# Optimization experiments

Measured on AMD Instinct MI355X. Metric: run time of the kernel, lower is better.

The kernel has to match this reference:

```python
import jax, jax.numpy as jnp
import numpy as np


def setup_inputs() -> dict:
    key = jax.random.key(0)
    k1, k2 = jax.random.split(key)
    N, D = 8192, 1024
    x = jax.random.normal(k1, (N, D), dtype=jnp.float32)
    w = jax.random.normal(k2, (D, 1), dtype=jnp.float32)
    return {"x": x, "w": w}


def reference(x, w):
    # x: [N, D], w: [D, 1]
    N = x.shape[0]
    a = jax.nn.sigmoid(x @ w)[:, 0]          # [N], values in (0, 1)
    b = jnp.cumsum(a)                         # [N] running sum
    idx = jnp.floor(b).astype(jnp.int32)      # bin index per column
    prev = jnp.concatenate([jnp.zeros(1, jnp.int32), idx[:-1]])
    same = idx == prev                        # did we stay in the same bin?
    frac = b - idx.astype(b.dtype)            # portion falling into bin `idx`
    cols = jnp.arange(N)
    # value written at [idx, i]: a_i if same bin, else the fractional overflow
    main_val = jnp.where(same, a, frac)
    # cross-boundary remainder written at [idx-1, i]
    cross_val = jnp.where(same, 0.0, a - frac)
    cross_row = jnp.where(same, idx, idx - 1)  # dummy (add 0) when same
    trans_mat = (
        jnp.zeros((N, N), dtype=x.dtype)
        .at[idx, cols].set(main_val)
        .at[cross_row, cols].add(cross_val)
    )
    return trans_mat @ x                      # [N, D]
```

## Files before the change

kernel.cpp:

```cpp
#include <hip/hip_runtime.h>
#include <math.h>


__global__ __launch_bounds__(256) void dot_sigmoid_kernel(
    const float* __restrict__ x, const float* __restrict__ w,
    float* __restrict__ a, double* __restrict__ blocksum,
    int* __restrict__ rowptr, int N, int D) {
  __shared__ float was[4];
  int t = threadIdx.x;
  int lane = t & 63;
  int wave = t >> 6;
  int row = blockIdx.x * 4 + wave;
  const float4* xr = reinterpret_cast<const float4*>(x + (size_t)row * D);
  const float4* w4 = reinterpret_cast<const float4*>(w);
  float acc = 0.f;
  int nv = D >> 2;
  for (int j = lane; j < nv; j += 64) {
    float4 xv = xr[j];
    float4 wv = w4[j];
    acc = fmaf(xv.x, wv.x, acc);
    acc = fmaf(xv.y, wv.y, acc);
    acc = fmaf(xv.z, wv.z, acc);
    acc = fmaf(xv.w, wv.w, acc);
  }
#pragma unroll
  for (int off = 32; off > 0; off >>= 1) acc += __shfl_down(acc, off, 64);
  if (lane == 0) {
    float av = 1.0f / (1.0f + expf(-acc));
    a[row] = av;
    was[wave] = av;
  }
  int gtid = blockIdx.x * 256 + t;
  if (gtid <= N) rowptr[gtid] = N;
  __syncthreads();
  if (t == 0)
    blocksum[blockIdx.x] =
        (double)was[0] + (double)was[1] + (double)was[2] + (double)was[3];
}

__global__ __launch_bounds__(256) void scan_emit_kernel(
    const float* __restrict__ a, const double* __restrict__ blocksum,
    float* __restrict__ mainv, float* __restrict__ crossv,
    int* __restrict__ rowptr, int N) {
  __shared__ double sg[256];
  __shared__ double wtot[4];
  int b = blockIdx.x;
  int t = threadIdx.x;
  int lane = t & 63;
  int wid = t >> 6;

  double g = 0.0;
#pragma unroll
  for (int j = 0; j < 8; ++j) g += blocksum[8 * t + j];
  double vg = g;
  for (int off = 1; off < 64; off <<= 1) {
    double n = __shfl_up(vg, off, 64);
    if (lane >= off) vg += n;
  }
  if (lane == 63) wtot[wid] = vg;
  __syncthreads();
  double wb = 0.0;
  for (int q = 0; q < wid; ++q) wb += wtot[q];
  sg[t] = wb + vg - g;
  __syncthreads();

  int i = b * 256 + t;
  float ai = a[i];
  double va = (double)ai;
  for (int off = 1; off < 64; off <<= 1) {
    double n = __shfl_up(va, off, 64);
    if (lane >= off) va += n;
  }
  double E = va - (double)ai;
  int g0 = lane & ~31;
  double Eg0 = __shfl(E, g0, 64);
  int gg = 8 * b + (t >> 5);
  double prevbd = sg[gg] + (E - Eg0);
  double bd = prevbd + (double)ai;
  float bf = (float)bd;
  float pf = (float)prevbd;
  int k = (int)floorf(bf);
  int kp = (int)floorf(pf);
  float frac = bf - (float)k;
  bool same = (k == kp);
  mainv[i] = same ? ai : frac;
  crossv[i] = same ? 0.f : (ai - frac);
  if (!same) rowptr[k] = i;
  if (b == 0 && t == 0) rowptr[0] = 0;
}

__global__ __launch_bounds__(256) void out_kernel(
    const float* __restrict__ x, const float* __restrict__ mainv,
    const float* __restrict__ crossv, const int* __restrict__ rowptr,
    float* __restrict__ out, int N, int D) {
  int t = threadIdx.x;
  int lane = t & 63;
  int wave = t >> 6;
  int r = blockIdx.x * 4 + wave;
  int nv = D >> 2;
  int q = nv >> 2;
  int s0 = rowptr[r];
  int s1 = rowptr[r + 1];
  const float4* xb = reinterpret_cast<const float4*>(x) + lane;
  float4 acc0 = make_float4(0.f, 0.f, 0.f, 0.f);
  float4 acc1 = acc0, acc2 = acc0, acc3 = acc0;
#define FMA4(A, W, V)      \
  A.x = fmaf(W, V.x, A.x); \
  A.y = fmaf(W, V.y, A.y); \
  A.z = fmaf(W, V.z, A.z); \
  A.w = fmaf(W, V.w, A.w);
  int i = s0;
  for (; i + 2 <= s1; i += 2) {
    float w0 = mainv[i];
    float w1 = mainv[i + 1];
    const float4* p0 = xb + (size_t)i * nv;
    const float4* p1 = p0 + nv;
    float4 a0 = p0[0], a1 = p0[q], a2 = p0[2 * q], a3 = p0[3 * q];
    float4 b0 = p1[0], b1 = p1[q], b2 = p1[2 * q], b3 = p1[3 * q];
    FMA4(acc0, w0, a0);
    FMA4(acc1, w0, a1);
    FMA4(acc2, w0, a2);
    FMA4(acc3, w0, a3);
    FMA4(acc0, w1, b0);
    FMA4(acc1, w1, b1);
    FMA4(acc2, w1, b2);
    FMA4(acc3, w1, b3);
  }
  if (i < s1) {
    float w0 = mainv[i];
    const float4* p0 = xb + (size_t)i * nv;
    float4 a0 = p0[0], a1 = p0[q], a2 = p0[2 * q], a3 = p0[3 * q];
    FMA4(acc0, w0, a0);
    FMA4(acc1, w0, a1);
    FMA4(acc2, w0, a2);
    FMA4(acc3, w0, a3);
  }
  if (s1 < N) {
    float wc = crossv[s1];
    const float4* p0 = xb + (size_t)s1 * nv;
    float4 a0 = p0[0], a1 = p0[q], a2 = p0[2 * q], a3 = p0[3 * q];
    FMA4(acc0, wc, a0);
    FMA4(acc1, wc, a1);
    FMA4(acc2, wc, a2);
    FMA4(acc3, wc, a3);
  }
#undef FMA4
  float4* ob = reinterpret_cast<float4*>(out + (size_t)r * D) + lane;
  ob[0] = acc0;
  ob[q] = acc1;
  ob[2 * q] = acc2;
  ob[3 * q] = acc3;
}

extern "C" void kernel_launch(void* const* d_in, const int* in_sizes, int n_in,
                              void* d_out, int out_size, void* d_ws, size_t ws_size,
                              hipStream_t stream) {
  const float* x = (const float*)d_in[0];
  const float* w = (const float*)d_in[1];
  float* out = (float*)d_out;
  int D = in_sizes[1];
  int N = in_sizes[0] / D;

  float* a = (float*)d_ws;
  float* mainv = a + N;
  float* crossv = mainv + N;
  int* rowptr = (int*)(crossv + N);
  double* blocksum = (double*)(((uintptr_t)(rowptr + N + 1) + 15) & ~15ull);

  hipLaunchKernelGGL(dot_sigmoid_kernel, dim3(N / 4), dim3(256), 0, stream,
                     x, w, a, blocksum, rowptr, N, D);
  hipLaunchKernelGGL(scan_emit_kernel, dim3(N / 256), dim3(256), 0, stream,
                     a, blocksum, mainv, crossv, rowptr, N);
  hipLaunchKernelGGL(out_kernel, dim3(N / 4), dim3(256), 0, stream,
                     x, mainv, crossv, rowptr, out, N, D);
}
```

Before: 93.61 us.

## Fuse scan and output kernels by binary-searching bin boundaries per row

```diff
diff --git a/kernel.cpp b/kernel.cpp
--- a/kernel.cpp
+++ b/kernel.cpp
@@ -4,8 +4,7 @@
 
 __global__ __launch_bounds__(256) void dot_sigmoid_kernel(
     const float* __restrict__ x, const float* __restrict__ w,
-    float* __restrict__ a, double* __restrict__ blocksum,
-    int* __restrict__ rowptr, int N, int D) {
+    float* __restrict__ a, double* __restrict__ blocksum, int N, int D) {
   __shared__ float was[4];
   int t = threadIdx.x;
   int lane = t & 63;
@@ -30,77 +29,84 @@
     a[row] = av;
     was[wave] = av;
   }
-  int gtid = blockIdx.x * 256 + t;
-  if (gtid <= N) rowptr[gtid] = N;
   __syncthreads();
   if (t == 0)
     blocksum[blockIdx.x] =
         (double)was[0] + (double)was[1] + (double)was[2] + (double)was[3];
 }
 
-__global__ __launch_bounds__(256) void scan_emit_kernel(
-    const float* __restrict__ a, const double* __restrict__ blocksum,
-    float* __restrict__ mainv, float* __restrict__ crossv,
-    int* __restrict__ rowptr, int N) {
-  __shared__ double sg[256];
-  __shared__ double wtot[4];
-  int b = blockIdx.x;
+__global__ __launch_bounds__(256) void scan_out_kernel(
+    const float* __restrict__ x, const float* __restrict__ a,
+    const double* __restrict__ blocksum, float* __restrict__ out,
+    int N, int D) {
+  __shared__ double Pb[2048];
+  __shared__ double wt[4];
   int t = threadIdx.x;
   int lane = t & 63;
   int wid = t >> 6;
+  int NB = N >> 2;
 
-  double g = 0.0;
+  double cj[8];
+  double run = 0.0;
 #pragma unroll
-  for (int j = 0; j < 8; ++j) g += blocksum[8 * t + j];
+  for (int j = 0; j < 8; ++j) {
+    run += blocksum[8 * t + j];
+    cj[j] = run;
+  }
+  double g = run;
   double vg = g;
   for (int off = 1; off < 64; off <<= 1) {
     double n = __shfl_up(vg, off, 64);
     if (lane >= off) vg += n;
   }
-  if (lane == 63) wtot[wid] = vg;
+  if (lane == 63) wt[wid] = vg;
   __syncthreads();
   double wb = 0.0;
-  for (int q = 0; q < wid; ++q) wb += wtot[q];
-  sg[t] = wb + vg - g;
+  for (int qq = 0; qq < wid; ++qq) wb += wt[qq];
+  double texcl = wb + (vg - g);
+#pragma unroll
+  for (int j = 0; j < 8; ++j) Pb[8 * t + j] = texcl + cj[j];
   __syncthreads();
 
-  int i = b * 256 + t;
-  float ai = a[i];
-  double va = (double)ai;
-  for (int off = 1; off < 64; off <<= 1) {
-    double n = __shfl_up(va, off, 64);
-    if (lane >= off) va += n;
+  int r = blockIdx.x * 4 + wid;
+  int s[2];
+  float bf[2];
+#pragma unroll
+  for (int k = 0; k < 2; ++k) {
+    float rf = (float)(r + k);
+    if ((float)Pb[NB - 1] < rf) {
+      s[k] = N;
+      bf[k] = 0.f;
+    } else {
+      int lo = 0, hi = NB - 1;
+      while (lo < hi) {
+        int mid = (lo + hi) >> 1;
+        if ((float)Pb[mid] >= rf) hi = mid;
+        else lo = mid + 1;
+      }
+      double bb = lo ? Pb[lo - 1] : 0.0;
+      int found = (lo << 2) + 3;
+      float bfv = 0.f;
+      bool done = false;
+#pragma unroll
+      for (int cc = 0; cc < 4; ++cc) {
+        bb += (double)a[(lo << 2) + cc];
+        if (!done) {
+          bfv = (float)bb;
+          if (bfv >= rf) {
+            found = (lo << 2) + cc;
+            done = true;
+          }
+        }
+      }
+      s[k] = found;
+      bf[k] = bfv;
+    }
   }
-  double E = va - (double)ai;
-  int g0 = lane & ~31;
-  double Eg0 = __shfl(E, g0, 64);
-  int gg = 8 * b + (t >> 5);
-  double prevbd = sg[gg] + (E - Eg0);
-  double bd = prevbd + (double)ai;
-  float bf = (float)bd;
-  float pf = (float)prevbd;
-  int k = (int)floorf(bf);
-  int kp = (int)floorf(pf);
-  float frac = bf - (float)k;
-  bool same = (k == kp);
-  mainv[i] = same ? ai : frac;
-  crossv[i] = same ? 0.f : (ai - frac);
-  if (!same) rowptr[k] = i;
-  if (b == 0 && t == 0) rowptr[0] = 0;
-}
+  int s0 = s[0], s1 = s[1];
 
-__global__ __launch_bounds__(256) void out_kernel(
-    const float* __restrict__ x, const float* __restrict__ mainv,
-    const float* __restrict__ crossv, const int* __restrict__ rowptr,
-    float* __restrict__ out, int N, int D) {
-  int t = threadIdx.x;
-  int lane = t & 63;
-  int wave = t >> 6;
-  int r = blockIdx.x * 4 + wave;
   int nv = D >> 2;
   int q = nv >> 2;
-  int s0 = rowptr[r];
-  int s1 = rowptr[r + 1];
   const float4* xb = reinterpret_cast<const float4*>(x) + lane;
   float4 acc0 = make_float4(0.f, 0.f, 0.f, 0.f);
   float4 acc1 = acc0, acc2 = acc0, acc3 = acc0;
@@ -109,10 +115,26 @@
   A.y = fmaf(W, V.y, A.y); \
   A.z = fmaf(W, V.z, A.z); \
   A.w = fmaf(W, V.w, A.w);
-  int i = s0;
+#define ADDCOL(I, W)                                  \
+  {                                                   \
+    const float4* p = xb + (size_t)(I)*nv;            \
+    float4 v0 = p[0], v1 = p[q], v2 = p[2 * q], v3 = p[3 * q]; \
+    FMA4(acc0, W, v0);                                \
+    FMA4(acc1, W, v1);                                \
+    FMA4(acc2, W, v2);                                \
+    FMA4(acc3, W, v3);                                \
+  }
+
+  int start = s0;
+  if (r > 0 && s0 < N) {
+    float fr0 = bf[0] - floorf(bf[0]);
+    ADDCOL(s0, fr0);
+    start = s0 + 1;
+  }
+  int i = start;
   for (; i + 2 <= s1; i += 2) {
-    float w0 = mainv[i];
-    float w1 = mainv[i + 1];
+    float w0 = a[i];
+    float w1 = a[i + 1];
     const float4* p0 = xb + (size_t)i * nv;
     const float4* p1 = p0 + nv;
     float4 a0 = p0[0], a1 = p0[q], a2 = p0[2 * q], a3 = p0[3 * q];
@@ -127,23 +149,15 @@
     FMA4(acc3, w1, b3);
   }
   if (i < s1) {
-    float w0 = mainv[i];
-    const float4* p0 = xb + (size_t)i * nv;
-    float4 a0 = p0[0], a1 = p0[q], a2 = p0[2 * q], a3 = p0[3 * q];
-    FMA4(acc0, w0, a0);
-    FMA4(acc1, w0, a1);
-    FMA4(acc2, w0, a2);
-    FMA4(acc3, w0, a3);
+    float w0 = a[i];
+    ADDCOL(i, w0);
   }
   if (s1 < N) {
-    float wc = crossv[s1];
-    const float4* p0 = xb + (size_t)s1 * nv;
-    float4 a0 = p0[0], a1 = p0[q], a2 = p0[2 * q], a3 = p0[3 * q];
-    FMA4(acc0, wc, a0);
-    FMA4(acc1, wc, a1);
-    FMA4(acc2, wc, a2);
-    FMA4(acc3, wc, a3);
+    float fr1 = bf[1] - floorf(bf[1]);
+    float wc = a[s1] - fr1;
+    ADDCOL(s1, wc);
   }
+#undef ADDCOL
 #undef FMA4
   float4* ob = reinterpret_cast<float4*>(out + (size_t)r * D) + lane;
   ob[0] = acc0;
@@ -162,15 +176,10 @@
   int N = in_sizes[0] / D;
 
   float* a = (float*)d_ws;
-  float* mainv = a + N;
-  float* crossv = mainv + N;
-  int* rowptr = (int*)(crossv + N);
-  double* blocksum = (double*)(((uintptr_t)(rowptr + N + 1) + 15) & ~15ull);
+  double* blocksum = (double*)(((uintptr_t)(a + N) + 15) & ~15ull);
 
   hipLaunchKernelGGL(dot_sigmoid_kernel, dim3(N / 4), dim3(256), 0, stream,
-                     x, w, a, blocksum, rowptr, N, D);
-  hipLaunchKernelGGL(scan_emit_kernel, dim3(N / 256), dim3(256), 0, stream,
-                     a, blocksum, mainv, crossv, rowptr, N);
-  hipLaunchKernelGGL(out_kernel, dim3(N / 4), dim3(256), 0, stream,
-                     x, mainv, crossv, rowptr, out, N, D);
+                     x, w, a, blocksum, N, D);
+  hipLaunchKernelGGL(scan_out_kernel, dim3(N / 4), dim3(256), 0, stream,
+                     x, a, blocksum, out, N, D);
 }
```

Measured after the change: 95.52 us. +2.0%, slower.
